# Performance work log

Measured on AMD Instinct MI355X. Metric: run time of the kernel, lower is better.

Reference implementation:

```python
import jax, jax.numpy as jnp
import numpy as np

B = 16      # number of point clouds in the batch
N = 2048    # points per cloud
P = B * N   # total points (flat PyG-style batching)
K = 16      # neighbors per point (col 0 = self loop)
OUT = 512   # out_channels


def _linear(key, fi, fo):
    # torch nn.Linear default init: U(-1/sqrt(fi), 1/sqrt(fi))
    s = 1.0 / np.sqrt(fi)
    kw, kb = jax.random.split(key)
    W = jax.random.uniform(kw, (fi, fo), jnp.float32, -s, s)
    b = jax.random.uniform(kb, (fo,), jnp.float32, -s, s)
    return W, b


def setup_inputs() -> dict:
    key = jax.random.key(0)
    ks = jax.random.split(key, 6)
    pos = jax.random.normal(ks[0], (P, 3), jnp.float32)
    # flat batch vector: points are grouped contiguously per cloud
    batch = (jnp.arange(P, dtype=jnp.int32) // N).astype(jnp.int32)
    # within-cloud random neighbor indices (stand-in for knn/radius graph)
    base = (jnp.arange(P) // N) * N  # offset of each point's cloud
    nbr = base[:, None] + jax.random.randint(ks[1], (P, K), 0, N)
    nbr = nbr.at[:, 0].set(jnp.arange(P))  # self loop (PyG add_self_loops)
    W1, b1 = _linear(ks[2], 3, 64)          # sa1 MLP layer 1
    W2, b2 = _linear(ks[3], 64, 128)        # sa1 MLP layer 2
    W3, b3 = _linear(ks[4], 128 + 3, 256)   # sa2 MLP layer 1
    W4, b4 = _linear(ks[5], 256, OUT)       # sa2 MLP layer 2
    return dict(pos=pos, nbr=nbr.astype(jnp.int64), batch=batch,
                W1=W1, b1=b1, W2=W2, b2=b2, W3=W3, b3=b3, W4=W4, b4=b4)


def reference(pos, nbr, batch, W1, b1, W2, b2, W3, b3, W4, b4):
    # ----- sa1: x is None -> message = MLP(pos_j - pos_i), max-aggregated -----
    diff = pos[nbr] - pos[:, None, :]                      # [P, K, 3]
    h1 = jnp.maximum(diff @ W1 + b1, 0.0) @ W2 + b2        # [P, K, 128]
    x1 = jnp.max(h1, axis=1)                               # [P, 128]
    # ----- sa2: message = MLP([x1_j, pos_j - pos_i]), max-aggregated -----
    feats = jnp.concatenate([x1[nbr], diff], axis=-1)      # [P, K, 131]
    h2 = jnp.maximum(feats @ W3 + b3, 0.0) @ W4 + b4       # [P, K, 512]
    x2 = jnp.max(h2, axis=1)                               # [P, 512]
    # ----- global_max_pool over batch -----
    return jax.ops.segment_max(x2, batch, num_segments=B)  # [B, 512]
```

## Files before the change

### kernel.cpp

```cpp
#include <hip/hip_runtime.h>
#include <hip/hip_bf16.h>

#define PTOT   32768
#define KNB    16
#define NCLOUD 16
#define OUTC   512
#define A1S    168
#define A2S    264

typedef __attribute__((ext_vector_type(8)))  short v8bf;
typedef __attribute__((ext_vector_type(16))) float v16f;

__device__ __forceinline__ unsigned short f2b(float v) {
    __hip_bfloat16 h = __float2bfloat16(v);
    return *reinterpret_cast<unsigned short*>(&h);
}
__device__ __forceinline__ unsigned pk2(float a, float b) {
    return (unsigned)f2b(a) | ((unsigned)f2b(b) << 16);
}
__device__ __forceinline__ unsigned fenc(float f) {
    unsigned u = __float_as_uint(f);
    return (u & 0x80000000u) ? ~u : (u | 0x80000000u);
}
__device__ __forceinline__ float fdec(unsigned u) {
    unsigned b = (u & 0x80000000u) ? (u & 0x7FFFFFFFu) : ~u;
    return __uint_as_float(b);
}
__device__ __forceinline__ v16f zero16() {
    v16f z;
    #pragma unroll
    for (int i = 0; i < 16; ++i) z[i] = 0.0f;
    return z;
}

__global__ void prep_kernel(const float* __restrict__ W1, const float* __restrict__ W2,
                            const float* __restrict__ W3, const float* __restrict__ W4,
                            unsigned short* __restrict__ W1s, unsigned short* __restrict__ W2s,
                            unsigned short* __restrict__ W3s, unsigned short* __restrict__ W4s,
                            unsigned* __restrict__ encbuf)
{
    int i = blockIdx.x * 256 + threadIdx.x;
    if (i < NCLOUD * OUTC) encbuf[i] = 0u;
    if (i < 40960) {
        int j = i & 7, n = (i >> 3) & 255, c2 = i >> 11;
        int k = c2 * 8 + j;
        W3s[i] = f2b(k < 131 ? W3[k * 256 + n] : 0.0f);
    }
    int i2 = i - 40960;
    if (i2 >= 0 && i2 < 131072) {
        int j = i2 & 7, n = (i2 >> 3) & 511, c2 = i2 >> 12;
        int k = c2 * 8 + j;
        W4s[i2] = f2b(W4[k * 512 + n]);
    }
    int i3 = i - 172032;
    if (i3 >= 0 && i3 < 1024) {
        int k = i3 & 15, n = i3 >> 4;
        W1s[i3] = f2b(k < 3 ? W1[k * 64 + n] : 0.0f);
    }
    int i4 = i - 173056;
    if (i4 >= 0 && i4 < 8192) {
        int k = i4 & 63, n = i4 >> 6;
        W2s[i4] = f2b(W2[k * 128 + n]);
    }
}

__global__ __launch_bounds__(256) void sa1_kernel(
    const float* __restrict__ pos, const int* __restrict__ nbr,
    const unsigned short* __restrict__ W1s, const float* __restrict__ b1,
    const unsigned short* __restrict__ W2s, const float* __restrict__ b2,
    unsigned short* __restrict__ x1b)
{
    __shared__ unsigned short A1d[64 * 16];
    __shared__ unsigned short A2[64 * 72];
    const int tid  = threadIdx.x;
    const int lane = tid & 63;
    const int wave = tid >> 6;
    const int l31  = lane & 31;
    const int h    = lane >> 5;

    const int c1 = (wave >> 1) * 32 + l31;
    const v8bf b1f = *(const v8bf*)(W1s + c1 * 16 + h * 8);
    const float b1v = b1[c1];
    v8bf B2[4];
    #pragma unroll
    for (int kc = 0; kc < 4; ++kc)
        B2[kc] = *(const v8bf*)(W2s + (wave * 32 + l31) * 64 + kc * 16 + h * 8);
    const float b2v = b2[wave * 32 + l31];

    #pragma unroll
    for (int g = 0; g < 2; ++g) {
        const int p0 = blockIdx.x * 8 + g * 4;
        __syncthreads();
        if (tid < 64) {
            int r = tid;
            int j = nbr[p0 * KNB + r];
            int p = p0 + (r >> 4);
            v8bf z;
            #pragma unroll
            for (int i = 0; i < 8; ++i) z[i] = 0;
            v8bf dv = z;
            dv[0] = (short)f2b(pos[j * 3 + 0] - pos[p * 3 + 0]);
            dv[1] = (short)f2b(pos[j * 3 + 1] - pos[p * 3 + 1]);
            dv[2] = (short)f2b(pos[j * 3 + 2] - pos[p * 3 + 2]);
            *(v8bf*)(A1d + r * 16)     = dv;
            *(v8bf*)(A1d + r * 16 + 8) = z;
        }
        __syncthreads();

        {
            v8bf a = *(const v8bf*)(A1d + ((wave & 1) * 32 + l31) * 16 + h * 8);
            v16f acc = __builtin_amdgcn_mfma_f32_32x32x16_bf16(a, b1f, zero16(), 0, 0, 0);
            #pragma unroll
            for (int r = 0; r < 16; ++r) {
                int row = (wave & 1) * 32 + (r & 3) + 8 * (r >> 2) + 4 * h;
                A2[row * 72 + c1] = f2b(fmaxf(acc[r] + b1v, 0.0f));
            }
        }
        __syncthreads();

        #pragma unroll
        for (int rt = 0; rt < 2; ++rt) {
            v16f acc = zero16();
            #pragma unroll
            for (int kc = 0; kc < 4; ++kc) {
                v8bf a = *(const v8bf*)(A2 + (rt * 32 + l31) * 72 + kc * 16 + h * 8);
                acc = __builtin_amdgcn_mfma_f32_32x32x16_bf16(a, B2[kc], acc, 0, 0, 0);
            }
            float ma = acc[0], mb = acc[8];
            #pragma unroll
            for (int r = 1; r < 8; ++r) { ma = fmaxf(ma, acc[r]); mb = fmaxf(mb, acc[8 + r]); }
            ma = fmaxf(ma, __shfl_xor(ma, 32));
            mb = fmaxf(mb, __shfl_xor(mb, 32));
            int p = p0 + rt * 2 + h;
            float m = h ? mb : ma;
            x1b[p * 128 + wave * 32 + l31] = f2b(m + b2v);
        }
    }
}

__global__ __launch_bounds__(256) void sa2_kernel(
    const float* __restrict__ pos, const int* __restrict__ nbr,
    const int* __restrict__ batch,
    const unsigned short* __restrict__ W3s, const float* __restrict__ b3,
    const unsigned short* __restrict__ W4s, const float* __restrict__ b4,
    const unsigned short* __restrict__ x1b, unsigned* __restrict__ encbuf)
{
    __shared__ unsigned short S[128 * A2S];
    const int tid  = threadIdx.x;
    const int lane = tid & 63;
    const int wave = tid >> 6;
    const int l31  = lane & 31;
    const int h    = lane >> 5;
    const int p0   = blockIdx.x * 8;

    const float b3v0 = b3[(wave * 2 + 0) * 32 + l31];
    const float b3v1 = b3[(wave * 2 + 1) * 32 + l31];

    {
        int r = tid >> 1, q = tid & 1;
        int j = nbr[p0 * KNB + r];
        const uint4* src = (const uint4*)(x1b + j * 128 + q * 64);
        uint4* dst = (uint4*)(S + r * A1S + q * 64);
        #pragma unroll
        for (int i = 0; i < 8; ++i) dst[i] = src[i];
    }
    if (tid < 128) {
        int r = tid;
        int j = nbr[p0 * KNB + r];
        int p = p0 + (r >> 4);
        v8bf z;
        #pragma unroll
        for (int i = 0; i < 8; ++i) z[i] = 0;
        v8bf dv = z;
        dv[0] = (short)f2b(pos[j * 3 + 0] - pos[p * 3 + 0]);
        dv[1] = (short)f2b(pos[j * 3 + 1] - pos[p * 3 + 1]);
        dv[2] = (short)f2b(pos[j * 3 + 2] - pos[p * 3 + 2]);
        *(v8bf*)(S + r * A1S + 128) = dv;
        *(v8bf*)(S + r * A1S + 136) = z;
    }
    __syncthreads();

    const int n1a = (wave * 2 + 0) * 32 + l31;
    const int n1b = (wave * 2 + 1) * 32 + l31;
    unsigned stA[2][16], stB[2][16];
    #pragma unroll
    for (int rtp = 0; rtp < 2; ++rtp) {
        v16f g00 = zero16(), g01 = zero16(), g10 = zero16(), g11 = zero16();
        #pragma unroll
        for (int kc = 0; kc < 9; ++kc) {
            v8bf a0 = *(const v8bf*)(S + (rtp * 64 + l31)      * A1S + kc * 16 + h * 8);
            v8bf a1 = *(const v8bf*)(S + (rtp * 64 + 32 + l31) * A1S + kc * 16 + h * 8);
            int c2 = kc * 2 + h;
            v8bf B0 = *(const v8bf*)(W3s + ((c2 * 256 + n1a) << 3));
            v8bf B1 = *(const v8bf*)(W3s + ((c2 * 256 + n1b) << 3));
            g00 = __builtin_amdgcn_mfma_f32_32x32x16_bf16(a0, B0, g00, 0, 0, 0);
            g10 = __builtin_amdgcn_mfma_f32_32x32x16_bf16(a1, B0, g10, 0, 0, 0);
            g01 = __builtin_amdgcn_mfma_f32_32x32x16_bf16(a0, B1, g01, 0, 0, 0);
            g11 = __builtin_amdgcn_mfma_f32_32x32x16_bf16(a1, B1, g11, 0, 0, 0);
        }
        #pragma unroll
        for (int i = 0; i < 8; ++i) {
            stA[rtp][i]     = pk2(fmaxf(g00[2*i] + b3v0, 0.0f), fmaxf(g00[2*i+1] + b3v0, 0.0f));
            stA[rtp][8 + i] = pk2(fmaxf(g10[2*i] + b3v0, 0.0f), fmaxf(g10[2*i+1] + b3v0, 0.0f));
            stB[rtp][i]     = pk2(fmaxf(g01[2*i] + b3v1, 0.0f), fmaxf(g01[2*i+1] + b3v1, 0.0f));
            stB[rtp][8 + i] = pk2(fmaxf(g11[2*i] + b3v1, 0.0f), fmaxf(g11[2*i+1] + b3v1, 0.0f));
        }
    }
    __syncthreads();

    {
        const int c0 = (wave * 2 + 0) * 32 + l31;
        const int c1 = (wave * 2 + 1) * 32 + l31;
        #pragma unroll
        for (int rtp = 0; rtp < 2; ++rtp) {
            const int rb = rtp * 64;
            #pragma unroll
            for (int i = 0; i < 8; ++i) {
                int row = rb + ((2*i) & 3) + 8 * ((2*i) >> 2) + 4 * h;
                S[row * A2S + c0]        = (unsigned short)(stA[rtp][i] & 0xFFFF);
                S[(row + 1) * A2S + c0]  = (unsigned short)(stA[rtp][i] >> 16);
                S[(row + 32) * A2S + c0] = (unsigned short)(stA[rtp][8 + i] & 0xFFFF);
                S[(row + 33) * A2S + c0] = (unsigned short)(stA[rtp][8 + i] >> 16);
                S[row * A2S + c1]        = (unsigned short)(stB[rtp][i] & 0xFFFF);
                S[(row + 1) * A2S + c1]  = (unsigned short)(stB[rtp][i] >> 16);
                S[(row + 32) * A2S + c1] = (unsigned short)(stB[rtp][8 + i] & 0xFFFF);
                S[(row + 33) * A2S + c1] = (unsigned short)(stB[rtp][8 + i] >> 16);
            }
        }
    }
    __syncthreads();

    const int cloud = batch[p0];
    #pragma unroll
    for (int cp = 0; cp < 2; ++cp) {
        const int ct0 = wave * 4 + cp * 2;
        const int n0 = ct0 * 32 + l31;
        const int n1 = (ct0 + 1) * 32 + l31;
        v8bf B2a[16], B2b[16];
        #pragma unroll
        for (int kc = 0; kc < 16; ++kc) {
            int c2 = kc * 2 + h;
            B2a[kc] = *(const v8bf*)(W4s + ((c2 * 512 + n0) << 3));
            B2b[kc] = *(const v8bf*)(W4s + ((c2 * 512 + n1) << 3));
        }
        float rm0 = -3.4e38f, rm1 = -3.4e38f;
        #pragma unroll
        for (int rtp = 0; rtp < 2; ++rtp) {
            v16f a00 = zero16(), a01 = zero16(), a10 = zero16(), a11 = zero16();
            #pragma unroll
            for (int kc = 0; kc < 16; ++kc) {
                v8bf a0 = *(const v8bf*)(S + (rtp * 64 + l31)      * A2S + kc * 16 + h * 8);
                v8bf a1 = *(const v8bf*)(S + (rtp * 64 + 32 + l31) * A2S + kc * 16 + h * 8);
                a00 = __builtin_amdgcn_mfma_f32_32x32x16_bf16(a0, B2a[kc], a00, 0, 0, 0);
                a10 = __builtin_amdgcn_mfma_f32_32x32x16_bf16(a1, B2a[kc], a10, 0, 0, 0);
                a01 = __builtin_amdgcn_mfma_f32_32x32x16_bf16(a0, B2b[kc], a01, 0, 0, 0);
                a11 = __builtin_amdgcn_mfma_f32_32x32x16_bf16(a1, B2b[kc], a11, 0, 0, 0);
            }
            #pragma unroll
            for (int r = 0; r < 16; ++r) {
                rm0 = fmaxf(rm0, fmaxf(a00[r], a10[r]));
                rm1 = fmaxf(rm1, fmaxf(a01[r], a11[r]));
            }
        }
        rm0 = fmaxf(rm0, __shfl_xor(rm0, 32));
        rm1 = fmaxf(rm1, __shfl_xor(rm1, 32));
        rm0 += b4[ct0 * 32 + l31];
        rm1 += b4[(ct0 + 1) * 32 + l31];
        if (lane < 32) {
            atomicMax(&encbuf[cloud * OUTC + ct0 * 32 + l31], fenc(rm0));
            atomicMax(&encbuf[cloud * OUTC + (ct0 + 1) * 32 + l31], fenc(rm1));
        }
    }
}

__global__ void finalize_kernel(const unsigned* __restrict__ encv,
                                float* __restrict__ out)
{
    int i = blockIdx.x * 256 + threadIdx.x;
    if (i < NCLOUD * OUTC) out[i] = fdec(encv[i]);
}

extern "C" void kernel_launch(void* const* d_in, const int* in_sizes, int n_in,
                              void* d_out, int out_size, void* d_ws, size_t ws_size,
                              hipStream_t stream)
{
    const float* pos   = (const float*)d_in[0];
    const int*   nbr   = (const int*)  d_in[1];
    const int*   batch = (const int*)  d_in[2];
    const float* W1    = (const float*)d_in[3];
    const float* b1    = (const float*)d_in[4];
    const float* W2    = (const float*)d_in[5];
    const float* b2    = (const float*)d_in[6];
    const float* W3    = (const float*)d_in[7];
    const float* b3    = (const float*)d_in[8];
    const float* W4    = (const float*)d_in[9];
    const float* b4    = (const float*)d_in[10];

    unsigned short* x1b = (unsigned short*)d_ws;
    unsigned short* W3s = (unsigned short*)((char*)d_ws + 8388608);
    unsigned short* W4s = (unsigned short*)((char*)d_ws + 8470528);
    unsigned*    encbuf = (unsigned*)((char*)d_ws + 8732672);
    unsigned short* W1s = (unsigned short*)((char*)d_ws + 8765440);
    unsigned short* W2s = (unsigned short*)((char*)d_ws + 8767488);

    prep_kernel<<<708, 256, 0, stream>>>(W1, W2, W3, W4, W1s, W2s, W3s, W4s, encbuf);
    sa1_kernel<<<PTOT / 8, 256, 0, stream>>>(pos, nbr, W1s, b1, W2s, b2, x1b);
    sa2_kernel<<<PTOT / 8, 256, 0, stream>>>(pos, nbr, batch, W3s, b3, W4s, b4, x1b, encbuf);
    finalize_kernel<<<(NCLOUD * OUTC + 255) / 256, 256, 0, stream>>>(encbuf, (float*)d_out);
}
```

Before: 251.2 us.

## Fold weight prep into sa1 and finalize into sa2 via last-block counter

Removes the separate prep and finalize kernels. The W3/W4 bf16 repacking and the zeroing of encbuf and the counter now run at the start of sa1 blocks. W1 and W2 are read from fp32 and converted per block in registers. The final decode runs in whichever sa2 block is last to increment an atomic counter, after a threadfence. This cuts two kernel launches and their gaps, at the cost of strided fp32 W2 loads in every sa1 block and a fence plus atomic per sa2 block.

```diff
diff --git a/kernel.cpp b/kernel.cpp
--- a/kernel.cpp
+++ b/kernel.cpp
@@ -33,41 +33,13 @@
     return z;
 }
 
-__global__ void prep_kernel(const float* __restrict__ W1, const float* __restrict__ W2,
-                            const float* __restrict__ W3, const float* __restrict__ W4,
-                            unsigned short* __restrict__ W1s, unsigned short* __restrict__ W2s,
-                            unsigned short* __restrict__ W3s, unsigned short* __restrict__ W4s,
-                            unsigned* __restrict__ encbuf)
-{
-    int i = blockIdx.x * 256 + threadIdx.x;
-    if (i < NCLOUD * OUTC) encbuf[i] = 0u;
-    if (i < 40960) {
-        int j = i & 7, n = (i >> 3) & 255, c2 = i >> 11;
-        int k = c2 * 8 + j;
-        W3s[i] = f2b(k < 131 ? W3[k * 256 + n] : 0.0f);
-    }
-    int i2 = i - 40960;
-    if (i2 >= 0 && i2 < 131072) {
-        int j = i2 & 7, n = (i2 >> 3) & 511, c2 = i2 >> 12;
-        int k = c2 * 8 + j;
-        W4s[i2] = f2b(W4[k * 512 + n]);
-    }
-    int i3 = i - 172032;
-    if (i3 >= 0 && i3 < 1024) {
-        int k = i3 & 15, n = i3 >> 4;
-        W1s[i3] = f2b(k < 3 ? W1[k * 64 + n] : 0.0f);
-    }
-    int i4 = i - 173056;
-    if (i4 >= 0 && i4 < 8192) {
-        int k = i4 & 63, n = i4 >> 6;
-        W2s[i4] = f2b(W2[k * 128 + n]);
-    }
-}
-
 __global__ __launch_bounds__(256) void sa1_kernel(
     const float* __restrict__ pos, const int* __restrict__ nbr,
-    const unsigned short* __restrict__ W1s, const float* __restrict__ b1,
-    const unsigned short* __restrict__ W2s, const float* __restrict__ b2,
+    const float* __restrict__ W1, const float* __restrict__ b1,
+    const float* __restrict__ W2, const float* __restrict__ b2,
+    const float* __restrict__ W3, const float* __restrict__ W4,
+    unsigned short* __restrict__ W3s, unsigned short* __restrict__ W4s,
+    unsigned* __restrict__ encbuf, unsigned* __restrict__ ctr,
     unsigned short* __restrict__ x1b)
 {
     __shared__ unsigned short A1d[64 * 16];
@@ -78,14 +50,43 @@
     const int l31  = lane & 31;
     const int h    = lane >> 5;
 
+    {
+        int ip = blockIdx.x * 256 + tid;
+        if (ip < 40960) {
+            int j = ip & 7, n = (ip >> 3) & 255, c2 = ip >> 11;
+            int k = c2 * 8 + j;
+            W3s[ip] = f2b(k < 131 ? W3[k * 256 + n] : 0.0f);
+        }
+        int i2 = ip - 40960;
+        if (i2 >= 0 && i2 < 131072) {
+            int j = i2 & 7, n = (i2 >> 3) & 511, c2 = i2 >> 12;
+            int k = c2 * 8 + j;
+            W4s[i2] = f2b(W4[k * 512 + n]);
+        }
+        if (blockIdx.x == 4095) {
+            for (int i = tid; i < NCLOUD * OUTC; i += 256) encbuf[i] = 0u;
+            if (tid == 0) *ctr = 0u;
+        }
+    }
+
     const int c1 = (wave >> 1) * 32 + l31;
-    const v8bf b1f = *(const v8bf*)(W1s + c1 * 16 + h * 8);
+    v8bf b1f;
+    #pragma unroll
+    for (int i = 0; i < 8; ++i) b1f[i] = 0;
+    if (h == 0) {
+        b1f[0] = (short)f2b(W1[c1]);
+        b1f[1] = (short)f2b(W1[64 + c1]);
+        b1f[2] = (short)f2b(W1[128 + c1]);
+    }
     const float b1v = b1[c1];
+    const int cW2 = wave * 32 + l31;
     v8bf B2[4];
     #pragma unroll
     for (int kc = 0; kc < 4; ++kc)
-        B2[kc] = *(const v8bf*)(W2s + (wave * 32 + l31) * 64 + kc * 16 + h * 8);
-    const float b2v = b2[wave * 32 + l31];
+        #pragma unroll
+        for (int j = 0; j < 8; ++j)
+            B2[kc][j] = (short)f2b(W2[(kc * 16 + h * 8 + j) * 128 + cW2]);
+    const float b2v = b2[cW2];
 
     #pragma unroll
     for (int g = 0; g < 2; ++g) {
@@ -143,7 +144,8 @@
     const int* __restrict__ batch,
     const unsigned short* __restrict__ W3s, const float* __restrict__ b3,
     const unsigned short* __restrict__ W4s, const float* __restrict__ b4,
-    const unsigned short* __restrict__ x1b, unsigned* __restrict__ encbuf)
+    const unsigned short* __restrict__ x1b, unsigned* __restrict__ encbuf,
+    unsigned* __restrict__ ctr, float* __restrict__ out)
 {
     __shared__ unsigned short S[128 * A2S];
     const int tid  = threadIdx.x;
@@ -271,13 +273,21 @@
             atomicMax(&encbuf[cloud * OUTC + (ct0 + 1) * 32 + l31], fenc(rm1));
         }
     }
-}
-
-__global__ void finalize_kernel(const unsigned* __restrict__ encv,
-                                float* __restrict__ out)
-{
-    int i = blockIdx.x * 256 + threadIdx.x;
-    if (i < NCLOUD * OUTC) out[i] = fdec(encv[i]);
+
+    __threadfence();
+    __syncthreads();
+    unsigned* flag = (unsigned*)S;
+    if (tid == 0) {
+        unsigned old = atomicAdd(ctr, 1u);
+        *flag = (old == gridDim.x - 1) ? 1u : 0u;
+    }
+    __syncthreads();
+    if (*flag) {
+        for (int i = tid; i < NCLOUD * OUTC; i += 256) {
+            unsigned e = atomicOr(&encbuf[i], 0u);
+            out[i] = fdec(e);
+        }
+    }
 }
 
 extern "C" void kernel_launch(void* const* d_in, const int* in_sizes, int n_in,
@@ -300,11 +310,10 @@
     unsigned short* W3s = (unsigned short*)((char*)d_ws + 8388608);
     unsigned short* W4s = (unsigned short*)((char*)d_ws + 8470528);
     unsigned*    encbuf = (unsigned*)((char*)d_ws + 8732672);
-    unsigned short* W1s = (unsigned short*)((char*)d_ws + 8765440);
-    unsigned short* W2s = (unsigned short*)((char*)d_ws + 8767488);
-
-    prep_kernel<<<708, 256, 0, stream>>>(W1, W2, W3, W4, W1s, W2s, W3s, W4s, encbuf);
-    sa1_kernel<<<PTOT / 8, 256, 0, stream>>>(pos, nbr, W1s, b1, W2s, b2, x1b);
-    sa2_kernel<<<PTOT / 8, 256, 0, stream>>>(pos, nbr, batch, W3s, b3, W4s, b4, x1b, encbuf);
-    finalize_kernel<<<(NCLOUD * OUTC + 255) / 256, 256, 0, stream>>>(encbuf, (float*)d_out);
-}
+    unsigned*       ctr = (unsigned*)((char*)d_ws + 8765440);
+
+    sa1_kernel<<<PTOT / 8, 256, 0, stream>>>(pos, nbr, W1, b1, W2, b2, W3, W4,
+                                             W3s, W4s, encbuf, ctr, x1b);
+    sa2_kernel<<<PTOT / 8, 256, 0, stream>>>(pos, nbr, batch, W3s, b3, W4s, b4,
+                                             x1b, encbuf, ctr, (float*)d_out);
+}
```

Result: slower. 507.2 us (+101.9%).
